# Kernel tuning notes

Hardware: AMD Instinct MI355X
Metric: run time of the kernel (lower is better)

## Reference

```python
import jax, jax.numpy as jnp
import numpy as np

N = 50000
E = 800000
IN_DIM = 128
HID = 128
OUT = 40


def setup_inputs() -> dict:
    key = jax.random.key(0)
    k1, k2, k3, k4, k5 = jax.random.split(key, 5)
    x = jax.random.normal(k1, (N, IN_DIM), dtype=jnp.float32)
    edge_index = jax.random.randint(k2, (2, E), 0, N, dtype=jnp.int64)
    # Glorot-ish init for GCNConv weights, zero bias (PyG default bias=True)
    W1 = jax.random.normal(k3, (IN_DIM, HID), dtype=jnp.float32) / np.sqrt(IN_DIM)
    b1 = jnp.zeros((HID,), dtype=jnp.float32)
    W2 = jax.random.normal(k4, (HID, OUT), dtype=jnp.float32) / np.sqrt(HID)
    b2 = jnp.zeros((OUT,), dtype=jnp.float32)
    return {"x": x, "edge_index": edge_index, "W1": W1, "b1": b1, "W2": W2, "b2": b2}


def _gcn_norm(edge_index, n_nodes):
    """Add self-loops and compute symmetric GCN normalization per edge.
    Returns (src, dst, norm) with len E + n_nodes."""
    loops = jnp.arange(n_nodes, dtype=edge_index.dtype)
    src = jnp.concatenate([edge_index[0], loops])
    dst = jnpp_concat = jnp.concatenate([edge_index[1], loops])
    dst = jnp.concatenate([edge_index[1], loops])
    deg = jax.ops.segment_sum(jnp.ones_like(dst, dtype=jnp.float32), dst,
                              num_segments=n_nodes)
    dinv = jnp.where(deg > 0, jax.lax.rsqrt(deg), 0.0)
    norm = dinv[src] * dinv[dst]  # [E + N]
    return src, dst, norm


def _gcn_conv(x, src, dst, norm, W, b, n_nodes):
    xw = x @ W                                  # [N, F_out] transform first
    msg = xw[src] * norm[:, None]               # gather + scale, [E+N, F_out]
    out = jax.ops.segment_sum(msg, dst, num_segments=n_nodes)  # scatter-add
    return out + b


def reference(x, edge_index, W1, b1, W2, b2):
    n = x.shape[0]
    src, dst, norm = _gcn_norm(edge_index, n)
    h = _gcn_conv(x, src, dst, norm, W1, b1, n)
    h = jax.nn.relu(h)
    # dropout is identity in eval mode (training=False)
    h = _gcn_conv(h, src, dst, norm, W2, b2, n)
    return jax.nn.softmax(h, axis=1)
```

## Files before the change

### kernel.cpp

```cpp
#include <hip/hip_runtime.h>
#include <hip/hip_fp16.h>

#define IN_DIM 128
#define HID    128
#define OUTC   40
#define CAP    64
#define LSTR   136

typedef _Float16 f16x8 __attribute__((ext_vector_type(8)));
typedef _Float16 f16x4 __attribute__((ext_vector_type(4)));
typedef float    f32x4 __attribute__((ext_vector_type(4)));
typedef int      i32x4 __attribute__((ext_vector_type(4)));

__device__ __forceinline__ int permi(int d, int NP8) { return (d & 7) * NP8 + (d >> 3); }

__global__ __launch_bounds__(256) void k_scatter(const int* __restrict__ edge, int* __restrict__ cnt,
                                                 unsigned short* __restrict__ col,
                                                 const float* __restrict__ W1, const float* __restrict__ W2,
                                                 _Float16* __restrict__ W1T, _Float16* __restrict__ W2T,
                                                 int E, int n, int nbS, int NP8) {
  int b = blockIdx.x;
  if (b >= nbS) {
    int t = (b - nbS) * 256 + threadIdx.x;
    if (t < 128 * 128) {
      int nn = t >> 7, kk = t & 127;
      W1T[t] = (_Float16)W1[kk * 128 + nn];
    }
    if (t < 48 * 128) {
      int nn = t >> 7, kk = t & 127;
      W2T[t] = (nn < OUTC) ? (_Float16)W2[kk * OUTC + nn] : (_Float16)0.f;
    }
    return;
  }
  int g = b & 7;
  auto proc = [&](int d, int s) {
    if ((d & 7) != g || (unsigned)d >= (unsigned)n || (unsigned)s >= (unsigned)n) return;
    int p   = g * NP8 + (d >> 3);
    int pos = atomicAdd(&cnt[p], 1);
    if (pos < CAP) col[(size_t)p * CAP + pos] = (unsigned short)s;
  };
  int t       = (b >> 3) * 256 + threadIdx.x;
  int gstride = (nbS >> 3) * 256;
  int E4      = E >> 2;
  const i32x4* srcv = (const i32x4*)edge;
  const i32x4* dstv = (const i32x4*)&edge[E];
  for (int q = t; q < E4; q += gstride) {
    i32x4 dq = __builtin_nontemporal_load(&dstv[q]);
    i32x4 sq = __builtin_nontemporal_load(&srcv[q]);
    proc(dq[0], sq[0]); proc(dq[1], sq[1]); proc(dq[2], sq[2]); proc(dq[3], sq[3]);
  }
  if (b == 0) {
    for (int e = E4 * 4 + threadIdx.x; e < E; e += 256) {
      int d  = edge[E + e];
      int sv = edge[e];
      if ((unsigned)d >= (unsigned)n || (unsigned)sv >= (unsigned)n) continue;
      int p   = (d & 7) * NP8 + (d >> 3);
      int pos = atomicAdd(&cnt[p], 1);
      if (pos < CAP) col[(size_t)p * CAP + pos] = (unsigned short)sv;
    }
  }
}


__global__ __launch_bounds__(256) void k_gemm1(const float* __restrict__ x, const _Float16* __restrict__ W1T,
                                               const int* __restrict__ cnt, __half* __restrict__ xws,
                                               int n, int NP8) {
  __shared__ _Float16 sW[128 * LSTR];
  __shared__ _Float16 sX[64 * LSTR];
  int tid = threadIdx.x;
  int i0  = blockIdx.x * 64;

  {
    const uint4* src = (const uint4*)W1T;
    for (int idx = tid; idx < 2048; idx += 256) {
      int nn = idx >> 4, c = idx & 15;
      *(uint4*)&sW[nn * LSTR + c * 8] = src[nn * 16 + c];
    }
  }
  for (int idx = tid; idx < 2048; idx += 256) {
    int r = idx >> 5, c = idx & 31;
    int row = i0 + r;
    float4 v = (row < n) ? *(const float4*)&x[(size_t)row * IN_DIM + c * 4]
                         : make_float4(0.f, 0.f, 0.f, 0.f);
    f16x4 hv; hv[0] = (_Float16)v.x; hv[1] = (_Float16)v.y; hv[2] = (_Float16)v.z; hv[3] = (_Float16)v.w;
    *(f16x4*)&sX[r * LSTR + c * 4] = hv;
  }
  __syncthreads();

  int wv = tid >> 6, lane = tid & 63;
  int m = lane & 15, quad = lane >> 4;

  const _Float16* ax = &sX[(16 * wv + m) * LSTR + quad * 8];
  f16x8 a0 = *(const f16x8*)(ax);
  f16x8 a1 = *(const f16x8*)(ax + 32);
  f16x8 a2 = *(const f16x8*)(ax + 64);
  f16x8 a3 = *(const f16x8*)(ax + 96);

  int base_row = i0 + 16 * wv + quad * 4;
  float dvr[4];
#pragma unroll
  for (int r = 0; r < 4; ++r) {
    int row = base_row + r;
    dvr[r] = (row < n) ? rsqrtf((float)(cnt[permi(row, NP8)] + 1)) : 0.f;
  }

#pragma unroll
  for (int t = 0; t < 8; ++t) {
    const _Float16* bx = &sW[(t * 16 + m) * LSTR + quad * 8];
    f16x8 b0 = *(const f16x8*)(bx);
    f16x8 b1 = *(const f16x8*)(bx + 32);
    f16x8 b2 = *(const f16x8*)(bx + 64);
    f16x8 b3 = *(const f16x8*)(bx + 96);
    f32x4 c = {0.f, 0.f, 0.f, 0.f};
    c = __builtin_amdgcn_mfma_f32_16x16x32_f16(a0, b0, c, 0, 0, 0);
    c = __builtin_amdgcn_mfma_f32_16x16x32_f16(a1, b1, c, 0, 0, 0);
    c = __builtin_amdgcn_mfma_f32_16x16x32_f16(a2, b2, c, 0, 0, 0);
    c = __builtin_amdgcn_mfma_f32_16x16x32_f16(a3, b3, c, 0, 0, 0);
    int colb = t * 16 + m;
#pragma unroll
    for (int r = 0; r < 4; ++r) {
      int row = base_row + r;
      if (row < n) xws[(size_t)row * HID + colb] = __float2half(c[r] * dvr[r]);
    }
  }
}


__global__ __launch_bounds__(256) void k_agg1(const uint2* __restrict__ xws2, const int* __restrict__ cnt,
                                              const unsigned short* __restrict__ col, const float* __restrict__ b1,
                                              uint2* __restrict__ hv, int n, int NP8) {
  int wvid = (blockIdx.x * 256 + threadIdx.x) >> 6;
  int lane = threadIdx.x & 63;
  int half = lane >> 5;
  int f    = lane & 31;
  int wid  = wvid * 2 + half;
  if (wid >= n) return;
  uint2 sv = xws2[(size_t)wid * 32 + f];
  float2 alo = __half22float2(*(__half2*)&sv.x);
  float2 ahi = __half22float2(*(__half2*)&sv.y);
  int p   = permi(wid, NP8);
  int deg = cnt[p];
  int end = min(deg, CAP);
  const unsigned short* cp = &col[(size_t)p * CAP];
  int e = 0;
  for (; e + 4 <= end; e += 4) {
    int s0 = cp[e], s1 = cp[e+1], s2 = cp[e+2], s3 = cp[e+3];
    uint2 v0 = xws2[(size_t)s0 * 32 + f];
    uint2 v1 = xws2[(size_t)s1 * 32 + f];
    uint2 v2 = xws2[(size_t)s2 * 32 + f];
    uint2 v3 = xws2[(size_t)s3 * 32 + f];
    float2 l0 = __half22float2(*(__half2*)&v0.x), h0 = __half22float2(*(__half2*)&v0.y);
    float2 l1 = __half22float2(*(__half2*)&v1.x), h1 = __half22float2(*(__half2*)&v1.y);
    float2 l2 = __half22float2(*(__half2*)&v2.x), h2 = __half22float2(*(__half2*)&v2.y);
    float2 l3 = __half22float2(*(__half2*)&v3.x), h3 = __half22float2(*(__half2*)&v3.y);
    alo.x += (l0.x + l1.x) + (l2.x + l3.x);
    alo.y += (l0.y + l1.y) + (l2.y + l3.y);
    ahi.x += (h0.x + h1.x) + (h2.x + h3.x);
    ahi.y += (h0.y + h1.y) + (h2.y + h3.y);
  }
  for (; e < end; ++e) {
    uint2 v = xws2[(size_t)cp[e] * 32 + f];
    float2 l = __half22float2(*(__half2*)&v.x), hh = __half22float2(*(__half2*)&v.y);
    alo.x += l.x; alo.y += l.y; ahi.x += hh.x; ahi.y += hh.y;
  }
  float dv = rsqrtf((float)(deg + 1));
  float4 bb = ((const float4*)b1)[f];
  __half2 o0 = __floats2half2_rn(fmaxf(alo.x * dv + bb.x, 0.f), fmaxf(alo.y * dv + bb.y, 0.f));
  __half2 o1 = __floats2half2_rn(fmaxf(ahi.x * dv + bb.z, 0.f), fmaxf(ahi.y * dv + bb.w, 0.f));
  uint2 o; o.x = *(unsigned*)&o0; o.y = *(unsigned*)&o1;
  hv[(size_t)wid * 32 + f] = o;
}


__global__ __launch_bounds__(256) void k_gemm2(const __half* __restrict__ h, const _Float16* __restrict__ W2T,
                                               const int* __restrict__ cnt, __half* __restrict__ out,
                                               int n, int NP8) {
  __shared__ _Float16 sW[48 * LSTR];
  __shared__ _Float16 sH[64 * LSTR];
  int tid = threadIdx.x;
  int i0  = blockIdx.x * 64;

  {
    const uint4* src = (const uint4*)W2T;
    for (int idx = tid; idx < 768; idx += 256) {
      int nn = idx >> 4, c = idx & 15;
      *(uint4*)&sW[nn * LSTR + c * 8] = src[nn * 16 + c];
    }
  }
  {
    const uint4* src = (const uint4*)h;
    for (int idx = tid; idx < 1024; idx += 256) {
      int r = idx >> 4, c = idx & 15;
      int row = i0 + r;
      uint4 v = (row < n) ? src[(size_t)row * 16 + c] : make_uint4(0u, 0u, 0u, 0u);
      *(uint4*)&sH[r * LSTR + c * 8] = v;
    }
  }
  __syncthreads();

  int wv = tid >> 6, lane = tid & 63;
  int m = lane & 15, quad = lane >> 4;

  const _Float16* ax = &sH[(16 * wv + m) * LSTR + quad * 8];
  f16x8 a0 = *(const f16x8*)(ax);
  f16x8 a1 = *(const f16x8*)(ax + 32);
  f16x8 a2 = *(const f16x8*)(ax + 64);
  f16x8 a3 = *(const f16x8*)(ax + 96);

  int base_row = i0 + 16 * wv + quad * 4;
  float dvr[4];
#pragma unroll
  for (int r = 0; r < 4; ++r) {
    int row = base_row + r;
    dvr[r] = (row < n) ? rsqrtf((float)(cnt[permi(row, NP8)] + 1)) : 0.f;
  }

#pragma unroll
  for (int t = 0; t < 3; ++t) {
    const _Float16* bx = &sW[(t * 16 + m) * LSTR + quad * 8];
    f16x8 b0 = *(const f16x8*)(bx);
    f16x8 b1 = *(const f16x8*)(bx + 32);
    f16x8 b2 = *(const f16x8*)(bx + 64);
    f16x8 b3 = *(const f16x8*)(bx + 96);
    f32x4 c = {0.f, 0.f, 0.f, 0.f};
    c = __builtin_amdgcn_mfma_f32_16x16x32_f16(a0, b0, c, 0, 0, 0);
    c = __builtin_amdgcn_mfma_f32_16x16x32_f16(a1, b1, c, 0, 0, 0);
    c = __builtin_amdgcn_mfma_f32_16x16x32_f16(a2, b2, c, 0, 0, 0);
    c = __builtin_amdgcn_mfma_f32_16x16x32_f16(a3, b3, c, 0, 0, 0);
    int colb = t * 16 + m;
    if (colb < OUTC) {
#pragma unroll
      for (int r = 0; r < 4; ++r) {
        int row = base_row + r;
        if (row < n) out[(size_t)row * OUTC + colb] = __float2half(c[r] * dvr[r]);
      }
    }
  }
}


__global__ __launch_bounds__(256) void k_agg2(const __half2* __restrict__ hw2, const int* __restrict__ cnt,
                                              const unsigned short* __restrict__ col, const float* __restrict__ b2,
                                              float* __restrict__ out, int n, int NP8) {
  int wpair = (blockIdx.x * 256 + threadIdx.x) >> 6;
  int lane  = threadIdx.x & 63;
  int half  = lane >> 5;
  int f     = lane & 31;
  int wid   = wpair * 2 + half;
  bool act  = (f < OUTC / 2) && (wid < n);
  int widc  = (wid < n) ? wid : 0;
  int li    = act ? f : 0;
  int p     = permi(widc, NP8);
  int deg   = (wid < n) ? cnt[p] : 0;
  float2 acc = act ? __half22float2(hw2[(size_t)widc * (OUTC / 2) + li]) : make_float2(0.f, 0.f);
  int end = min(deg, CAP);
  const unsigned short* cp = &col[(size_t)p * CAP];
  int e = 0;
  for (; e + 8 <= end; e += 8) {
    int s0 = cp[e], s1 = cp[e+1], s2 = cp[e+2], s3 = cp[e+3];
    int s4 = cp[e+4], s5 = cp[e+5], s6 = cp[e+6], s7 = cp[e+7];
    if (act) {
      float2 v0 = __half22float2(hw2[(size_t)s0 * (OUTC / 2) + li]);
      float2 v1 = __half22float2(hw2[(size_t)s1 * (OUTC / 2) + li]);
      float2 v2 = __half22float2(hw2[(size_t)s2 * (OUTC / 2) + li]);
      float2 v3 = __half22float2(hw2[(size_t)s3 * (OUTC / 2) + li]);
      float2 v4 = __half22float2(hw2[(size_t)s4 * (OUTC / 2) + li]);
      float2 v5 = __half22float2(hw2[(size_t)s5 * (OUTC / 2) + li]);
      float2 v6 = __half22float2(hw2[(size_t)s6 * (OUTC / 2) + li]);
      float2 v7 = __half22float2(hw2[(size_t)s7 * (OUTC / 2) + li]);
      acc.x += (v0.x + v1.x) + (v2.x + v3.x) + ((v4.x + v5.x) + (v6.x + v7.x));
      acc.y += (v0.y + v1.y) + (v2.y + v3.y) + ((v4.y + v5.y) + (v6.y + v7.y));
    }
  }
  for (; e < end; ++e) {
    int s = cp[e];
    if (act) {
      float2 v = __half22float2(hw2[(size_t)s * (OUTC / 2) + li]);
      acc.x += v.x; acc.y += v.y;
    }
  }
  float dvd = rsqrtf((float)(deg + 1));
  float2 bb = act ? ((const float2*)b2)[li] : make_float2(0.f, 0.f);
  float lx = act ? acc.x * dvd + bb.x : -1e30f;
  float ly = act ? acc.y * dvd + bb.y : -1e30f;
  float m = fmaxf(lx, ly);
#pragma unroll
  for (int o = 16; o > 0; o >>= 1) m = fmaxf(m, __shfl_xor(m, o, 32));
  float ex = act ? __expf(lx - m) : 0.f;
  float ey = act ? __expf(ly - m) : 0.f;
  float sum = ex + ey;
#pragma unroll
  for (int o = 16; o > 0; o >>= 1) sum += __shfl_xor(sum, o, 32);
  if (act) {
    float inv = 1.f / sum;
    ((float2*)out)[(size_t)wid * (OUTC / 2) + li] = make_float2(ex * inv, ey * inv);
  }
}


extern "C" void kernel_launch(void* const* d_in, const int* in_sizes, int n_in,
                              void* d_out, int out_size, void* d_ws, size_t ws_size,
                              hipStream_t stream) {
  const float* x    = (const float*)d_in[0];
  const int*   edge = (const int*)d_in[1];
  const float* W1   = (const float*)d_in[2];
  const float* b1   = (const float*)d_in[3];
  const float* W2   = (const float*)d_in[4];
  const float* b2   = (const float*)d_in[5];
  float* out = (float*)d_out;

  int N   = in_sizes[0] / IN_DIM;
  int E   = in_sizes[1] / 2;
  int NP8 = (N + 7) / 8;
  int NP  = NP8 * 8;

  char* ws = (char*)d_ws;
  size_t off = 0;
  auto carve = [&](size_t bytes) { char* p = ws + off; off = (off + bytes + 255) & ~(size_t)255; return p; };
  int*            cnt = (int*)carve((size_t)NP * 4);
  unsigned short* col = (unsigned short*)carve((size_t)NP * CAP * 2);
  _Float16*       W1T = (_Float16*)carve((size_t)128 * 128 * 2);
  _Float16*       W2T = (_Float16*)carve((size_t)48 * 128 * 2);
  __half*         xws = (__half*)carve((size_t)N * HID * 2);
  __half*         h   = (__half*)carve((size_t)N * HID * 2);
  __half*         hw  = xws;

  (void)hipMemsetAsync(cnt, 0, (size_t)NP * 4, stream);

  int nbS  = 1024;
  int nbG  = (N + 63) / 64;
  int nbA1 = ((N + 1) / 2 * 64 + 255) / 256;
  int nbA2 = nbA1;

  k_scatter<<<nbS + 64, 256, 0, stream>>>(edge, cnt, col, W1, W2, W1T, W2T, E, N, nbS, NP8);
  k_gemm1<<<nbG, 256, 0, stream>>>(x, W1T, cnt, xws, N, NP8);
  k_agg1<<<nbA1, 256, 0, stream>>>((const uint2*)xws, cnt, col, b1, (uint2*)h, N, NP8);
  k_gemm2<<<nbG, 256, 0, stream>>>(h, W2T, cnt, hw, N, NP8);
  k_agg2<<<nbA2, 256, 0, stream>>>((const __half2*)hw, cnt, col, b2, out, N, NP8);
}
```

Measured before the change: 203.4 us.

## Fuse edge scatter with GEMM1 and aggregation1 with GEMM2

The edge bucketing is merged into the first dense transform kernel, with edge blocks and persistent GEMM blocks interleaved in one grid. GEMM1 no longer scales by the destination degree, so it does not have to wait for the counts; the first aggregation now applies per-source rsqrt(deg) itself. Layer-1 aggregation is fused with the second GEMM through shared memory, which removes the h round-trip to global memory and the separate weight-transpose step. The cost is extra cnt gathers per edge and every block transposing W1 or W2 into LDS on its own, with scattered LDS writes.

New measurement: 230.2 us. 1.13x slower.

```diff
diff --git a/kernel.cpp b/kernel.cpp
--- a/kernel.cpp
+++ b/kernel.cpp
@@ -6,6 +6,8 @@
 #define OUTC   40
 #define CAP    64
 #define LSTR   136
+#define NBS    1024
+#define NBG1   256
 
 typedef _Float16 f16x8 __attribute__((ext_vector_type(8)));
 typedef _Float16 f16x4 __attribute__((ext_vector_type(4)));
@@ -14,198 +16,188 @@
 
 __device__ __forceinline__ int permi(int d, int NP8) { return (d & 7) * NP8 + (d >> 3); }
 
-__global__ __launch_bounds__(256) void k_scatter(const int* __restrict__ edge, int* __restrict__ cnt,
-                                                 unsigned short* __restrict__ col,
-                                                 const float* __restrict__ W1, const float* __restrict__ W2,
-                                                 _Float16* __restrict__ W1T, _Float16* __restrict__ W2T,
-                                                 int E, int n, int nbS, int NP8) {
-  int b = blockIdx.x;
-  if (b >= nbS) {
-    int t = (b - nbS) * 256 + threadIdx.x;
-    if (t < 128 * 128) {
-      int nn = t >> 7, kk = t & 127;
-      W1T[t] = (_Float16)W1[kk * 128 + nn];
-    }
-    if (t < 48 * 128) {
-      int nn = t >> 7, kk = t & 127;
-      W2T[t] = (nn < OUTC) ? (_Float16)W2[kk * OUTC + nn] : (_Float16)0.f;
+__device__ __forceinline__ f16x8 cvt8(f32x4 lo, f32x4 hi) {
+  f16x8 r;
+  r[0] = (_Float16)lo[0]; r[1] = (_Float16)lo[1]; r[2] = (_Float16)lo[2]; r[3] = (_Float16)lo[3];
+  r[4] = (_Float16)hi[0]; r[5] = (_Float16)hi[1]; r[6] = (_Float16)hi[2]; r[7] = (_Float16)hi[3];
+  return r;
+}
+
+__global__ __launch_bounds__(256) void k_scatter_gemm1(const int* __restrict__ edge, int* __restrict__ cnt,
+                                                       unsigned short* __restrict__ col,
+                                                       const float* __restrict__ x, const float* __restrict__ W1,
+                                                       __half* __restrict__ xws,
+                                                       int E, int n, int NP8, int nT) {
+  __shared__ _Float16 sW[128 * LSTR];
+  int b   = blockIdx.x;
+  int c40 = b / 40, r40 = b % 40;
+
+  if (r40 < 32) {
+    int g = b & 7;
+    auto proc = [&](int d, int s) {
+      if ((d & 7) != g || (unsigned)d >= (unsigned)n || (unsigned)s >= (unsigned)n) return;
+      int p   = g * NP8 + (d >> 3);
+      int pos = atomicAdd(&cnt[p], 1);
+      if (pos < CAP) col[(size_t)p * CAP + pos] = (unsigned short)s;
+    };
+    int j = c40 * 4 + (r40 >> 3);
+    int t = j * 256 + threadIdx.x;
+    const int gstride = (NBS >> 3) * 256;
+    int E4 = E >> 2;
+    const i32x4* srcv = (const i32x4*)edge;
+    const i32x4* dstv = (const i32x4*)&edge[E];
+    for (int q = t; q < E4; q += gstride) {
+      i32x4 dq = __builtin_nontemporal_load(&dstv[q]);
+      i32x4 sq = __builtin_nontemporal_load(&srcv[q]);
+      proc(dq[0], sq[0]); proc(dq[1], sq[1]); proc(dq[2], sq[2]); proc(dq[3], sq[3]);
+    }
+    if (b == 0) {
+      for (int e = E4 * 4 + threadIdx.x; e < E; e += 256) {
+        int d  = edge[E + e];
+        int sv = edge[e];
+        if ((unsigned)d >= (unsigned)n || (unsigned)sv >= (unsigned)n) continue;
+        int p   = (d & 7) * NP8 + (d >> 3);
+        int pos = atomicAdd(&cnt[p], 1);
+        if (pos < CAP) col[(size_t)p * CAP + pos] = (unsigned short)sv;
+      }
     }
     return;
   }
-  int g = b & 7;
-  auto proc = [&](int d, int s) {
-    if ((d & 7) != g || (unsigned)d >= (unsigned)n || (unsigned)s >= (unsigned)n) return;
-    int p   = g * NP8 + (d >> 3);
-    int pos = atomicAdd(&cnt[p], 1);
-    if (pos < CAP) col[(size_t)p * CAP + pos] = (unsigned short)s;
-  };
-  int t       = (b >> 3) * 256 + threadIdx.x;
-  int gstride = (nbS >> 3) * 256;
-  int E4      = E >> 2;
-  const i32x4* srcv = (const i32x4*)edge;
-  const i32x4* dstv = (const i32x4*)&edge[E];
-  for (int q = t; q < E4; q += gstride) {
-    i32x4 dq = __builtin_nontemporal_load(&dstv[q]);
-    i32x4 sq = __builtin_nontemporal_load(&srcv[q]);
-    proc(dq[0], sq[0]); proc(dq[1], sq[1]); proc(dq[2], sq[2]); proc(dq[3], sq[3]);
-  }
-  if (b == 0) {
-    for (int e = E4 * 4 + threadIdx.x; e < E; e += 256) {
-      int d  = edge[E + e];
-      int sv = edge[e];
-      if ((unsigned)d >= (unsigned)n || (unsigned)sv >= (unsigned)n) continue;
-      int p   = (d & 7) * NP8 + (d >> 3);
-      int pos = atomicAdd(&cnt[p], 1);
-      if (pos < CAP) col[(size_t)p * CAP + pos] = (unsigned short)sv;
-    }
-  }
-}
-
-
-__global__ __launch_bounds__(256) void k_gemm1(const float* __restrict__ x, const _Float16* __restrict__ W1T,
-                                               const int* __restrict__ cnt, __half* __restrict__ xws,
-                                               int n, int NP8) {
-  __shared__ _Float16 sW[128 * LSTR];
-  __shared__ _Float16 sX[64 * LSTR];
+
   int tid = threadIdx.x;
-  int i0  = blockIdx.x * 64;
-
   {
-    const uint4* src = (const uint4*)W1T;
-    for (int idx = tid; idx < 2048; idx += 256) {
-      int nn = idx >> 4, c = idx & 15;
-      *(uint4*)&sW[nn * LSTR + c * 8] = src[nn * 16 + c];
-    }
-  }
-  for (int idx = tid; idx < 2048; idx += 256) {
-    int r = idx >> 5, c = idx & 31;
-    int row = i0 + r;
-    float4 v = (row < n) ? *(const float4*)&x[(size_t)row * IN_DIM + c * 4]
-                         : make_float4(0.f, 0.f, 0.f, 0.f);
-    f16x4 hv; hv[0] = (_Float16)v.x; hv[1] = (_Float16)v.y; hv[2] = (_Float16)v.z; hv[3] = (_Float16)v.w;
-    *(f16x4*)&sX[r * LSTR + c * 4] = hv;
+    const f32x4* w4 = (const f32x4*)W1;
+    for (int idx = tid; idx < 4096; idx += 256) {
+      int kk = idx >> 5, nn4 = (idx & 31) * 4;
+      f32x4 v = w4[idx];
+      sW[(nn4 + 0) * LSTR + kk] = (_Float16)v[0];
+      sW[(nn4 + 1) * LSTR + kk] = (_Float16)v[1];
+      sW[(nn4 + 2) * LSTR + kk] = (_Float16)v[2];
+      sW[(nn4 + 3) * LSTR + kk] = (_Float16)v[3];
+    }
   }
   __syncthreads();
-
-  int wv = tid >> 6, lane = tid & 63;
-  int m = lane & 15, quad = lane >> 4;
-
-  const _Float16* ax = &sX[(16 * wv + m) * LSTR + quad * 8];
-  f16x8 a0 = *(const f16x8*)(ax);
-  f16x8 a1 = *(const f16x8*)(ax + 32);
-  f16x8 a2 = *(const f16x8*)(ax + 64);
-  f16x8 a3 = *(const f16x8*)(ax + 96);
-
-  int base_row = i0 + 16 * wv + quad * 4;
-  float dvr[4];
-#pragma unroll
-  for (int r = 0; r < 4; ++r) {
-    int row = base_row + r;
-    dvr[r] = (row < n) ? rsqrtf((float)(cnt[permi(row, NP8)] + 1)) : 0.f;
-  }
-
-#pragma unroll
-  for (int t = 0; t < 8; ++t) {
-    const _Float16* bx = &sW[(t * 16 + m) * LSTR + quad * 8];
-    f16x8 b0 = *(const f16x8*)(bx);
-    f16x8 b1 = *(const f16x8*)(bx + 32);
-    f16x8 b2 = *(const f16x8*)(bx + 64);
-    f16x8 b3 = *(const f16x8*)(bx + 96);
-    f32x4 c = {0.f, 0.f, 0.f, 0.f};
-    c = __builtin_amdgcn_mfma_f32_16x16x32_f16(a0, b0, c, 0, 0, 0);
-    c = __builtin_amdgcn_mfma_f32_16x16x32_f16(a1, b1, c, 0, 0, 0);
-    c = __builtin_amdgcn_mfma_f32_16x16x32_f16(a2, b2, c, 0, 0, 0);
-    c = __builtin_amdgcn_mfma_f32_16x16x32_f16(a3, b3, c, 0, 0, 0);
-    int colb = t * 16 + m;
-#pragma unroll
-    for (int r = 0; r < 4; ++r) {
-      int row = base_row + r;
-      if (row < n) xws[(size_t)row * HID + colb] = __float2half(c[r] * dvr[r]);
-    }
-  }
-}
-
-
-__global__ __launch_bounds__(256) void k_agg1(const uint2* __restrict__ xws2, const int* __restrict__ cnt,
-                                              const unsigned short* __restrict__ col, const float* __restrict__ b1,
-                                              uint2* __restrict__ hv, int n, int NP8) {
-  int wvid = (blockIdx.x * 256 + threadIdx.x) >> 6;
-  int lane = threadIdx.x & 63;
-  int half = lane >> 5;
-  int f    = lane & 31;
-  int wid  = wvid * 2 + half;
-  if (wid >= n) return;
-  uint2 sv = xws2[(size_t)wid * 32 + f];
-  float2 alo = __half22float2(*(__half2*)&sv.x);
-  float2 ahi = __half22float2(*(__half2*)&sv.y);
-  int p   = permi(wid, NP8);
-  int deg = cnt[p];
-  int end = min(deg, CAP);
-  const unsigned short* cp = &col[(size_t)p * CAP];
-  int e = 0;
-  for (; e + 4 <= end; e += 4) {
-    int s0 = cp[e], s1 = cp[e+1], s2 = cp[e+2], s3 = cp[e+3];
-    uint2 v0 = xws2[(size_t)s0 * 32 + f];
-    uint2 v1 = xws2[(size_t)s1 * 32 + f];
-    uint2 v2 = xws2[(size_t)s2 * 32 + f];
-    uint2 v3 = xws2[(size_t)s3 * 32 + f];
-    float2 l0 = __half22float2(*(__half2*)&v0.x), h0 = __half22float2(*(__half2*)&v0.y);
-    float2 l1 = __half22float2(*(__half2*)&v1.x), h1 = __half22float2(*(__half2*)&v1.y);
-    float2 l2 = __half22float2(*(__half2*)&v2.x), h2 = __half22float2(*(__half2*)&v2.y);
-    float2 l3 = __half22float2(*(__half2*)&v3.x), h3 = __half22float2(*(__half2*)&v3.y);
-    alo.x += (l0.x + l1.x) + (l2.x + l3.x);
-    alo.y += (l0.y + l1.y) + (l2.y + l3.y);
-    ahi.x += (h0.x + h1.x) + (h2.x + h3.x);
-    ahi.y += (h0.y + h1.y) + (h2.y + h3.y);
-  }
-  for (; e < end; ++e) {
-    uint2 v = xws2[(size_t)cp[e] * 32 + f];
-    float2 l = __half22float2(*(__half2*)&v.x), hh = __half22float2(*(__half2*)&v.y);
-    alo.x += l.x; alo.y += l.y; ahi.x += hh.x; ahi.y += hh.y;
-  }
-  float dv = rsqrtf((float)(deg + 1));
-  float4 bb = ((const float4*)b1)[f];
-  __half2 o0 = __floats2half2_rn(fmaxf(alo.x * dv + bb.x, 0.f), fmaxf(alo.y * dv + bb.y, 0.f));
-  __half2 o1 = __floats2half2_rn(fmaxf(ahi.x * dv + bb.z, 0.f), fmaxf(ahi.y * dv + bb.w, 0.f));
-  uint2 o; o.x = *(unsigned*)&o0; o.y = *(unsigned*)&o1;
-  hv[(size_t)wid * 32 + f] = o;
-}
-
-
-__global__ __launch_bounds__(256) void k_gemm2(const __half* __restrict__ h, const _Float16* __restrict__ W2T,
-                                               const int* __restrict__ cnt, __half* __restrict__ out,
-                                               int n, int NP8) {
+  int wv = tid >> 6, lane = tid & 63, m = lane & 15, quad = lane >> 4;
+  int bg = c40 * 8 + (r40 - 32);
+  for (int tile = bg; tile < nT; tile += NBG1) {
+    int i0   = tile * 64;
+    int arow = i0 + 16 * wv + m;
+    f16x8 a0, a1, a2, a3;
+    if (arow < n) {
+      const float* xr = &x[(size_t)arow * IN_DIM + quad * 8];
+      f32x4 u0 = __builtin_nontemporal_load((const f32x4*)(xr));
+      f32x4 u1 = __builtin_nontemporal_load((const f32x4*)(xr + 4));
+      f32x4 u2 = __builtin_nontemporal_load((const f32x4*)(xr + 32));
+      f32x4 u3 = __builtin_nontemporal_load((const f32x4*)(xr + 36));
+      f32x4 u4 = __builtin_nontemporal_load((const f32x4*)(xr + 64));
+      f32x4 u5 = __builtin_nontemporal_load((const f32x4*)(xr + 68));
+      f32x4 u6 = __builtin_nontemporal_load((const f32x4*)(xr + 96));
+      f32x4 u7 = __builtin_nontemporal_load((const f32x4*)(xr + 100));
+      a0 = cvt8(u0, u1); a1 = cvt8(u2, u3); a2 = cvt8(u4, u5); a3 = cvt8(u6, u7);
+    } else {
+#pragma unroll
+      for (int jj = 0; jj < 8; ++jj) {
+        a0[jj] = (_Float16)0.f; a1[jj] = (_Float16)0.f; a2[jj] = (_Float16)0.f; a3[jj] = (_Float16)0.f;
+      }
+    }
+    int base_row = i0 + 16 * wv + quad * 4;
+#pragma unroll
+    for (int t = 0; t < 8; ++t) {
+      const _Float16* bx = &sW[(t * 16 + m) * LSTR + quad * 8];
+      f16x8 bf0 = *(const f16x8*)(bx);
+      f16x8 bf1 = *(const f16x8*)(bx + 32);
+      f16x8 bf2 = *(const f16x8*)(bx + 64);
+      f16x8 bf3 = *(const f16x8*)(bx + 96);
+      f32x4 c = {0.f, 0.f, 0.f, 0.f};
+      c = __builtin_amdgcn_mfma_f32_16x16x32_f16(a0, bf0, c, 0, 0, 0);
+      c = __builtin_amdgcn_mfma_f32_16x16x32_f16(a1, bf1, c, 0, 0, 0);
+      c = __builtin_amdgcn_mfma_f32_16x16x32_f16(a2, bf2, c, 0, 0, 0);
+      c = __builtin_amdgcn_mfma_f32_16x16x32_f16(a3, bf3, c, 0, 0, 0);
+      int colb = t * 16 + m;
+#pragma unroll
+      for (int r = 0; r < 4; ++r) {
+        int row = base_row + r;
+        if (row < n) xws[(size_t)row * HID + colb] = __float2half(c[r]);
+      }
+    }
+  }
+}
+
+__global__ __launch_bounds__(256) void k_agg1_gemm2(const uint2* __restrict__ xws2, const int* __restrict__ cnt,
+                                                    const unsigned short* __restrict__ col,
+                                                    const float* __restrict__ b1, const float* __restrict__ W2,
+                                                    __half* __restrict__ hw, int n, int NP8) {
   __shared__ _Float16 sW[48 * LSTR];
   __shared__ _Float16 sH[64 * LSTR];
   int tid = threadIdx.x;
   int i0  = blockIdx.x * 64;
 
-  {
-    const uint4* src = (const uint4*)W2T;
-    for (int idx = tid; idx < 768; idx += 256) {
-      int nn = idx >> 4, c = idx & 15;
-      *(uint4*)&sW[nn * LSTR + c * 8] = src[nn * 16 + c];
-    }
-  }
-  {
-    const uint4* src = (const uint4*)h;
-    for (int idx = tid; idx < 1024; idx += 256) {
-      int r = idx >> 4, c = idx & 15;
-      int row = i0 + r;
-      uint4 v = (row < n) ? src[(size_t)row * 16 + c] : make_uint4(0u, 0u, 0u, 0u);
-      *(uint4*)&sH[r * LSTR + c * 8] = v;
-    }
+  for (int idx = tid; idx < 8192; idx += 256) {
+    int nn = idx & 63, kk = idx >> 6;
+    if (nn < 48) sW[nn * LSTR + kk] = (nn < OUTC) ? (_Float16)W2[kk * OUTC + nn] : (_Float16)0.f;
+  }
+
+  int hwid = tid >> 5, f = tid & 31;
+  float4 bb = ((const float4*)b1)[f];
+#pragma unroll 1
+  for (int it = 0; it < 8; ++it) {
+    int r   = it * 8 + hwid;
+    int row = i0 + r;
+    float ax = 0.f, ay = 0.f, az = 0.f, aw = 0.f;
+    if (row < n) {
+      int p     = permi(row, NP8);
+      int deg   = cnt[p];
+      float dvd = rsqrtf((float)(deg + 1));
+      uint2 sv  = xws2[(size_t)row * 32 + f];
+      float2 slo = __half22float2(*(__half2*)&sv.x);
+      float2 shi = __half22float2(*(__half2*)&sv.y);
+      ax = slo.x * dvd; ay = slo.y * dvd; az = shi.x * dvd; aw = shi.y * dvd;
+      int end = min(deg, CAP);
+      const unsigned short* cp = &col[(size_t)p * CAP];
+      int e = 0;
+      for (; e + 4 <= end; e += 4) {
+        int s0 = cp[e], s1 = cp[e + 1], s2 = cp[e + 2], s3 = cp[e + 3];
+        float d0 = rsqrtf((float)(cnt[permi(s0, NP8)] + 1));
+        float d1 = rsqrtf((float)(cnt[permi(s1, NP8)] + 1));
+        float d2 = rsqrtf((float)(cnt[permi(s2, NP8)] + 1));
+        float d3 = rsqrtf((float)(cnt[permi(s3, NP8)] + 1));
+        uint2 v0 = xws2[(size_t)s0 * 32 + f];
+        uint2 v1 = xws2[(size_t)s1 * 32 + f];
+        uint2 v2 = xws2[(size_t)s2 * 32 + f];
+        uint2 v3 = xws2[(size_t)s3 * 32 + f];
+        float2 l0 = __half22float2(*(__half2*)&v0.x), h0 = __half22float2(*(__half2*)&v0.y);
+        float2 l1 = __half22float2(*(__half2*)&v1.x), h1 = __half22float2(*(__half2*)&v1.y);
+        float2 l2 = __half22float2(*(__half2*)&v2.x), h2 = __half22float2(*(__half2*)&v2.y);
+        float2 l3 = __half22float2(*(__half2*)&v3.x), h3 = __half22float2(*(__half2*)&v3.y);
+        ax += l0.x * d0 + l1.x * d1 + l2.x * d2 + l3.x * d3;
+        ay += l0.y * d0 + l1.y * d1 + l2.y * d2 + l3.y * d3;
+        az += h0.x * d0 + h1.x * d1 + h2.x * d2 + h3.x * d3;
+        aw += h0.y * d0 + h1.y * d1 + h2.y * d2 + h3.y * d3;
+      }
+      for (; e < end; ++e) {
+        int s    = cp[e];
+        float dv = rsqrtf((float)(cnt[permi(s, NP8)] + 1));
+        uint2 v  = xws2[(size_t)s * 32 + f];
+        float2 l = __half22float2(*(__half2*)&v.x), hh = __half22float2(*(__half2*)&v.y);
+        ax += l.x * dv; ay += l.y * dv; az += hh.x * dv; aw += hh.y * dv;
+      }
+      ax = fmaxf(ax * dvd + bb.x, 0.f);
+      ay = fmaxf(ay * dvd + bb.y, 0.f);
+      az = fmaxf(az * dvd + bb.z, 0.f);
+      aw = fmaxf(aw * dvd + bb.w, 0.f);
+    }
+    f16x4 hv4;
+    hv4[0] = (_Float16)ax; hv4[1] = (_Float16)ay; hv4[2] = (_Float16)az; hv4[3] = (_Float16)aw;
+    *(f16x4*)&sH[r * LSTR + f * 4] = hv4;
   }
   __syncthreads();
 
-  int wv = tid >> 6, lane = tid & 63;
-  int m = lane & 15, quad = lane >> 4;
-
-  const _Float16* ax = &sH[(16 * wv + m) * LSTR + quad * 8];
-  f16x8 a0 = *(const f16x8*)(ax);
-  f16x8 a1 = *(const f16x8*)(ax + 32);
-  f16x8 a2 = *(const f16x8*)(ax + 64);
-  f16x8 a3 = *(const f16x8*)(ax + 96);
+  int wv = tid >> 6, lane = tid & 63, m = lane & 15, quad = lane >> 4;
+  const _Float16* axp = &sH[(16 * wv + m) * LSTR + quad * 8];
+  f16x8 a0 = *(const f16x8*)(axp);
+  f16x8 a1 = *(const f16x8*)(axp + 32);
+  f16x8 a2 = *(const f16x8*)(axp + 64);
+  f16x8 a3 = *(const f16x8*)(axp + 96);
 
   int base_row = i0 + 16 * wv + quad * 4;
   float dvr[4];
@@ -218,26 +210,25 @@
 #pragma unroll
   for (int t = 0; t < 3; ++t) {
     const _Float16* bx = &sW[(t * 16 + m) * LSTR + quad * 8];
-    f16x8 b0 = *(const f16x8*)(bx);
-    f16x8 b1 = *(const f16x8*)(bx + 32);
-    f16x8 b2 = *(const f16x8*)(bx + 64);
-    f16x8 b3 = *(const f16x8*)(bx + 96);
+    f16x8 bf0 = *(const f16x8*)(bx);
+    f16x8 bf1 = *(const f16x8*)(bx + 32);
+    f16x8 bf2 = *(const f16x8*)(bx + 64);
+    f16x8 bf3 = *(const f16x8*)(bx + 96);
     f32x4 c = {0.f, 0.f, 0.f, 0.f};
-    c = __builtin_amdgcn_mfma_f32_16x16x32_f16(a0, b0, c, 0, 0, 0);
-    c = __builtin_amdgcn_mfma_f32_16x16x32_f16(a1, b1, c, 0, 0, 0);
-    c = __builtin_amdgcn_mfma_f32_16x16x32_f16(a2, b2, c, 0, 0, 0);
-    c = __builtin_amdgcn_mfma_f32_16x16x32_f16(a3, b3, c, 0, 0, 0);
+    c = __builtin_amdgcn_mfma_f32_16x16x32_f16(a0, bf0, c, 0, 0, 0);
+    c = __builtin_amdgcn_mfma_f32_16x16x32_f16(a1, bf1, c, 0, 0, 0);
+    c = __builtin_amdgcn_mfma_f32_16x16x32_f16(a2, bf2, c, 0, 0, 0);
+    c = __builtin_amdgcn_mfma_f32_16x16x32_f16(a3, bf3, c, 0, 0, 0);
     int colb = t * 16 + m;
     if (colb < OUTC) {
 #pragma unroll
       for (int r = 0; r < 4; ++r) {
         int row = base_row + r;
-        if (row < n) out[(size_t)row * OUTC + colb] = __float2half(c[r] * dvr[r]);
-      }
-    }
-  }
-}
-
+        if (row < n) hw[(size_t)row * OUTC + colb] = __float2half(c[r] * dvr[r]);
+      }
+    }
+  }
+}
 
 __global__ __launch_bounds__(256) void k_agg2(const __half2* __restrict__ hw2, const int* __restrict__ cnt,
                                               const unsigned short* __restrict__ col, const float* __restrict__ b2,
@@ -319,22 +310,15 @@
   auto carve = [&](size_t bytes) { char* p = ws + off; off = (off + bytes + 255) & ~(size_t)255; return p; };
   int*            cnt = (int*)carve((size_t)NP * 4);
   unsigned short* col = (unsigned short*)carve((size_t)NP * CAP * 2);
-  _Float16*       W1T = (_Float16*)carve((size_t)128 * 128 * 2);
-  _Float16*       W2T = (_Float16*)carve((size_t)48 * 128 * 2);
   __half*         xws = (__half*)carve((size_t)N * HID * 2);
-  __half*         h   = (__half*)carve((size_t)N * HID * 2);
-  __half*         hw  = xws;
+  __half*         hw  = (__half*)carve((size_t)N * OUTC * 2);
 
   (void)hipMemsetAsync(cnt, 0, (size_t)NP * 4, stream);
 
-  int nbS  = 1024;
-  int nbG  = (N + 63) / 64;
-  int nbA1 = ((N + 1) / 2 * 64 + 255) / 256;
-  int nbA2 = nbA1;
-
-  k_scatter<<<nbS + 64, 256, 0, stream>>>(edge, cnt, col, W1, W2, W1T, W2T, E, N, nbS, NP8);
-  k_gemm1<<<nbG, 256, 0, stream>>>(x, W1T, cnt, xws, N, NP8);
-  k_agg1<<<nbA1, 256, 0, stream>>>((const uint2*)xws, cnt, col, b1, (uint2*)h, N, NP8);
-  k_gemm2<<<nbG, 256, 0, stream>>>(h, W2T, cnt, hw, N, NP8);
+  int nT   = (N + 63) / 64;
+  int nbA2 = ((N + 1) / 2 * 64 + 255) / 256;
+
+  k_scatter_gemm1<<<NBS + NBG1, 256, 0, stream>>>(edge, cnt, col, x, W1, xws, E, N, NP8, nT);
+  k_agg1_gemm2<<<nT, 256, 0, stream>>>((const uint2*)xws, cnt, col, b1, W2, hw, N, NP8);
   k_agg2<<<nbA2, 256, 0, stream>>>((const __half2*)hw, cnt, col, b2, out, N, NP8);
 }
```
